# Kernel tuning notes

Hardware: AMD Instinct MI355X
Metric: run time of the kernel (lower is better)

Reference implementation:

```python
import jax, jax.numpy as jnp
import numpy as np

B, C, H, W = 32, 32, 64, 64   # batch, in_channel, image height/width
HC = 1                        # hashtable channel groups (in_channel % HC == 0)
KS = 9                        # kernel_size: top-k neighbors per pixel
K = 64                        # kernel_number_per_pixel (output channels)
P = H * W                     # pixel_number


def setup_inputs() -> dict:
    key = jax.random.key(0)
    k1, k2, k3 = jax.random.split(key, 3)
    x = jax.random.normal(k1, (B, C, H, W), dtype=jnp.float32)
    # Per-pixel affinity scores -> top-KS neighbor indices (mimics
    # _build_full_hash: argsort descending, take first kernel_size).
    scores = jax.random.normal(k2, (HC, H, W, P), dtype=jnp.float32)
    idx = jnp.argsort(-scores, axis=-1)[..., :KS].astype(jnp.int32)  # (HC, NH, NW, KS)
    bound = float(np.sqrt(1.0 / (C * KS)))
    weights = jax.random.uniform(k3, (K, C * KS), minval=-bound, maxval=bound,
                                 dtype=jnp.float32)
    return {"x": x, "weights": weights, "idx": idx}


def reference(x, weights, idx):
    Bx, Cx, Hx, Wx = x.shape
    HCx, NH, NW, ks = idx.shape
    Px = Hx * Wx
    # full_hash[b, c, i, j, k] = idx[c % HC, i, j, k] + c*P + b*C*P,
    # so x.take(full_hash) == gather of x[b, c] at idx[c % HC].
    idx_full = jnp.tile(idx, (Cx // HCx, 1, 1, 1)).reshape(Cx, NH * NW * ks)
    g = jnp.take_along_axis(x.reshape(Bx, Cx, Px), idx_full[None], axis=2)  # (B, C, NH*NW*ks)
    # permute(1,4,0,2,3).reshape(C*ks, B*NH*NW)
    g = g.reshape(Bx, Cx, NH, NW, ks).transpose(1, 4, 0, 2, 3).reshape(Cx * ks, Bx * NH * NW)
    out = (weights @ g).reshape(-1, Bx, NH, NW)  # (K, B, NH, NW)
    return jnp.transpose(out, (1, 0, 2, 3))       # (B, K, NH, NW)
```

## Files before the change

kernel.cpp:

```cpp
#include <hip/hip_runtime.h>
#include <hip/hip_bf16.h>

#define BB 32
#define CC 32
#define PP 4096
#define KS 9
#define KK 64
#define CK 288

typedef __attribute__((ext_vector_type(8))) short short8;
typedef __attribute__((ext_vector_type(4))) float float4v;

__device__ inline unsigned short f2bf(float f) {
    __hip_bfloat16 h = __float2bfloat16(f);
    return __builtin_bit_cast(unsigned short, h);
}

__global__ __launch_bounds__(256)
void prep_kernel(const float* __restrict__ x, const float* __restrict__ w,
                 unsigned short* __restrict__ xt, unsigned short* __restrict__ wa) {
    const int t = threadIdx.x;
    const int blk = blockIdx.x;
    if (blk < 512) {
        const int b = blk >> 4;
        const int p = ((blk & 15) << 8) + t;
        const float* xb = x + (size_t)b * CC * PP + p;
        unsigned int buf[16];
#pragma unroll
        for (int c2 = 0; c2 < 16; ++c2) {
            float lo = xb[(size_t)(2 * c2) * PP];
            float hi = xb[(size_t)(2 * c2 + 1) * PP];
            buf[c2] = (unsigned int)f2bf(lo) | ((unsigned int)f2bf(hi) << 16);
        }
        uint4* dst = (uint4*)(xt + ((size_t)b * PP + p) * CC);
        const uint4* s = (const uint4*)buf;
#pragma unroll
        for (int j = 0; j < 4; ++j) dst[j] = s[j];
    } else {
        int i = (blk - 512) * 256 + t;
        if (i < KK * CK) {
            int j  = i & 7;
            int l  = (i >> 3) & 63;
            int mt = (i >> 9) & 3;
            int kc = i >> 11;
            int c  = ((l >> 4) << 3) + j;
            int ko = (mt << 4) + (l & 15);
            wa[i] = f2bf(w[ko * CK + c * KS + kc]);
        }
    }
}

__global__ __launch_bounds__(256)
void abc_mfma2_kernel(const unsigned short* __restrict__ xt,
                      const unsigned short* __restrict__ wa,
                      const int* __restrict__ idx,
                      float* __restrict__ out) {
    const int t    = threadIdx.x;
    const int l    = t & 63;
    const int w    = t >> 6;
    const int b    = blockIdx.x >> 5;
    const int p0   = ((blockIdx.x & 31) << 7) + (w << 5);
    const int lo16 = l & 15;
    const int quad = l >> 4;

    const unsigned short* xtb = xt + (size_t)b * PP * CC;

    float4v acc[8];
#pragma unroll
    for (int i = 0; i < 8; ++i) acc[i] = (float4v){0.f, 0.f, 0.f, 0.f};

#pragma unroll 3
    for (int kc = 0; kc < 9; ++kc) {
        short8 bf[2];
#pragma unroll
        for (int nt = 0; nt < 2; ++nt) {
            const int pl = p0 + nt * 16 + lo16;
            const int q  = idx[pl * KS + kc];
            bf[nt] = *(const short8*)(xtb + (size_t)q * CC + (quad << 3));
        }
        const short8* wf = (const short8*)(wa) + (kc * 4) * 64 + l;
#pragma unroll
        for (int mt = 0; mt < 4; ++mt) {
            short8 a = wf[mt * 64];
#pragma unroll
            for (int nt = 0; nt < 2; ++nt)
                acc[mt * 2 + nt] =
                    __builtin_amdgcn_mfma_f32_16x16x32_bf16(a, bf[nt], acc[mt * 2 + nt], 0, 0, 0);
        }
    }

    float* ob = out + (size_t)b * KK * PP + p0 + lo16;
#pragma unroll
    for (int mt = 0; mt < 4; ++mt) {
        float* om = ob + (size_t)(mt * 16 + quad * 4) * PP;
#pragma unroll
        for (int r = 0; r < 4; ++r)
#pragma unroll
            for (int nt = 0; nt < 2; ++nt)
                om[(size_t)r * PP + nt * 16] = acc[mt * 2 + nt][r];
    }
}

__global__ __launch_bounds__(256)
void abc_valu_kernel(const float* __restrict__ x, const float* __restrict__ w,
                     const int* __restrict__ idx, float* __restrict__ out) {
    __shared__ float xrow[PP];
    const int t = threadIdx.x;
    const int b = blockIdx.x >> 4;
    const int p = ((blockIdx.x & 15) << 8) + t;
    int q[KS];
#pragma unroll
    for (int k = 0; k < KS; ++k) q[k] = idx[p * KS + k];
    float acc[KK];
#pragma unroll
    for (int i = 0; i < KK; ++i) acc[i] = 0.0f;
    const float* xb = x + (size_t)b * CC * PP;
#pragma unroll 1
    for (int c = 0; c < CC; ++c) {
        const float4* src = (const float4*)(xb + (size_t)c * PP);
        float4* dst = (float4*)xrow;
#pragma unroll
        for (int j = 0; j < 4; ++j) dst[j * 256 + t] = src[j * 256 + t];
        __syncthreads();
        float xv[KS];
#pragma unroll
        for (int k = 0; k < KS; ++k) xv[k] = xrow[q[k]];
#pragma unroll
        for (int k = 0; k < KS; ++k) {
            const int col = c * KS + k;
#pragma unroll
            for (int ko = 0; ko < KK; ++ko)
                acc[ko] += xv[k] * w[ko * CK + col];
        }
        __syncthreads();
    }
    float* ob = out + (size_t)b * KK * PP + p;
#pragma unroll
    for (int ko = 0; ko < KK; ++ko)
        ob[(size_t)ko * PP] = acc[ko];
}

extern "C" void kernel_launch(void* const* d_in, const int* in_sizes, int n_in,
                              void* d_out, int out_size, void* d_ws, size_t ws_size,
                              hipStream_t stream) {
    const float* x  = (const float*)d_in[0];
    const float* w  = (const float*)d_in[1];
    const int* idx  = (const int*)d_in[2];
    float* out      = (float*)d_out;

    const size_t xt_bytes = (size_t)BB * PP * CC * 2;
    const size_t need     = xt_bytes + (size_t)KK * CK * 2;

    if (ws_size >= need) {
        unsigned short* xt = (unsigned short*)d_ws;
        unsigned short* wa = (unsigned short*)((char*)d_ws + xt_bytes);
        const int wb_blocks = (KK * CK + 255) / 256;
        prep_kernel<<<512 + wb_blocks, 256, 0, stream>>>(x, w, xt, wa);
        abc_mfma2_kernel<<<BB * (PP / 128), 256, 0, stream>>>(xt, wa, idx, out);
    } else {
        abc_valu_kernel<<<BB * (PP / 256), 256, 0, stream>>>(x, w, idx, out);
    }
}
```

Before: 96.97 us.

## Vectorize prep transpose, hoist idx loads, add occupancy hint and nontemporal stores

After: 99.23 us. 2.3% more time.

```diff
diff --git a/kernel.cpp b/kernel.cpp
--- a/kernel.cpp
+++ b/kernel.cpp
@@ -21,23 +21,30 @@
                  unsigned short* __restrict__ xt, unsigned short* __restrict__ wa) {
     const int t = threadIdx.x;
     const int blk = blockIdx.x;
-    if (blk < 512) {
-        const int b = blk >> 4;
-        const int p = ((blk & 15) << 8) + t;
-        const float* xb = x + (size_t)b * CC * PP + p;
-        unsigned int buf[16];
+    if (blk < 128) {
+        const int b  = blk >> 2;
+        const int p4 = (((blk & 3) << 8) + t) << 2;
+        const float* xb = x + (size_t)b * CC * PP + p4;
+        unsigned int rows[4][16];
 #pragma unroll
-        for (int c2 = 0; c2 < 16; ++c2) {
-            float lo = xb[(size_t)(2 * c2) * PP];
-            float hi = xb[(size_t)(2 * c2 + 1) * PP];
-            buf[c2] = (unsigned int)f2bf(lo) | ((unsigned int)f2bf(hi) << 16);
+        for (int c = 0; c < CC; c += 2) {
+            float4 v0 = *(const float4*)(xb + (size_t)c * PP);
+            float4 v1 = *(const float4*)(xb + (size_t)(c + 1) * PP);
+            const int cp = c >> 1;
+            rows[0][cp] = (unsigned int)f2bf(v0.x) | ((unsigned int)f2bf(v1.x) << 16);
+            rows[1][cp] = (unsigned int)f2bf(v0.y) | ((unsigned int)f2bf(v1.y) << 16);
+            rows[2][cp] = (unsigned int)f2bf(v0.z) | ((unsigned int)f2bf(v1.z) << 16);
+            rows[3][cp] = (unsigned int)f2bf(v0.w) | ((unsigned int)f2bf(v1.w) << 16);
         }
-        uint4* dst = (uint4*)(xt + ((size_t)b * PP + p) * CC);
-        const uint4* s = (const uint4*)buf;
 #pragma unroll
-        for (int j = 0; j < 4; ++j) dst[j] = s[j];
+        for (int j = 0; j < 4; ++j) {
+            uint4* dst = (uint4*)(xt + ((size_t)b * PP + p4 + j) * CC);
+            const uint4* s = (const uint4*)rows[j];
+#pragma unroll
+            for (int u = 0; u < 4; ++u) dst[u] = s[u];
+        }
     } else {
-        int i = (blk - 512) * 256 + t;
+        int i = (blk - 128) * 256 + t;
         if (i < KK * CK) {
             int j  = i & 7;
             int l  = (i >> 3) & 63;
@@ -50,7 +57,7 @@
     }
 }
 
-__global__ __launch_bounds__(256)
+__global__ __launch_bounds__(256, 4)
 void abc_mfma2_kernel(const unsigned short* __restrict__ xt,
                       const unsigned short* __restrict__ wa,
                       const int* __restrict__ idx,
@@ -65,19 +72,24 @@
 
     const unsigned short* xtb = xt + (size_t)b * PP * CC;
 
+    int q[2][KS];
+#pragma unroll
+    for (int nt = 0; nt < 2; ++nt) {
+        const int pl = p0 + nt * 16 + lo16;
+#pragma unroll
+        for (int kc = 0; kc < KS; ++kc) q[nt][kc] = idx[pl * KS + kc];
+    }
+
     float4v acc[8];
 #pragma unroll
     for (int i = 0; i < 8; ++i) acc[i] = (float4v){0.f, 0.f, 0.f, 0.f};
 
 #pragma unroll 3
-    for (int kc = 0; kc < 9; ++kc) {
+    for (int kc = 0; kc < KS; ++kc) {
         short8 bf[2];
 #pragma unroll
-        for (int nt = 0; nt < 2; ++nt) {
-            const int pl = p0 + nt * 16 + lo16;
-            const int q  = idx[pl * KS + kc];
-            bf[nt] = *(const short8*)(xtb + (size_t)q * CC + (quad << 3));
-        }
+        for (int nt = 0; nt < 2; ++nt)
+            bf[nt] = *(const short8*)(xtb + (size_t)q[nt][kc] * CC + (quad << 3));
         const short8* wf = (const short8*)(wa) + (kc * 4) * 64 + l;
 #pragma unroll
         for (int mt = 0; mt < 4; ++mt) {
@@ -97,7 +109,8 @@
         for (int r = 0; r < 4; ++r)
 #pragma unroll
             for (int nt = 0; nt < 2; ++nt)
-                om[(size_t)r * PP + nt * 16] = acc[mt * 2 + nt][r];
+                __builtin_nontemporal_store(acc[mt * 2 + nt][r],
+                                            om + (size_t)r * PP + nt * 16);
     }
 }
 
@@ -155,7 +168,7 @@
         unsigned short* xt = (unsigned short*)d_ws;
         unsigned short* wa = (unsigned short*)((char*)d_ws + xt_bytes);
         const int wb_blocks = (KK * CK + 255) / 256;
-        prep_kernel<<<512 + wb_blocks, 256, 0, stream>>>(x, w, xt, wa);
+        prep_kernel<<<128 + wb_blocks, 256, 0, stream>>>(x, w, xt, wa);
         abc_mfma2_kernel<<<BB * (PP / 128), 256, 0, stream>>>(xt, wa, idx, out);
     } else {
         abc_valu_kernel<<<BB * (PP / 256), 256, 0, stream>>>(x, w, idx, out);
```
